# Kernel tuning notes

Hardware: AMD Instinct MI355X
Metric: run time of the kernel (lower is better)

The kernel has to match this reference:

```python
import jax, jax.numpy as jnp
import numpy as np

HIDDEN = 1024
N_EXPERTS = 8
TOP_K = 2
INTER = 1408
NORM_TOPK = False


def setup_inputs() -> dict:
    key = jax.random.key(0)
    ks = jax.random.split(key, 5)
    B, S = 4, 2048
    scale_h = 1.0 / np.sqrt(HIDDEN)
    scale_i = 1.0 / np.sqrt(INTER)
    return {
        "hidden_states": jax.random.normal(ks[0], (B, S, HIDDEN), dtype=jnp.float32),
        "gate_w": jax.random.normal(ks[1], (N_EXPERTS, HIDDEN), dtype=jnp.float32) * scale_h,  # router
        "w_gate": jax.random.normal(ks[2], (N_EXPERTS, HIDDEN, INTER), dtype=jnp.float32) * scale_h,
        "w_up": jax.random.normal(ks[3], (N_EXPERTS, HIDDEN, INTER), dtype=jnp.float32) * scale_h,
        "w_down": jax.random.normal(ks[4], (N_EXPERTS, INTER, HIDDEN), dtype=jnp.float32) * scale_i,
    }


def reference(hidden_states, gate_w, w_gate, w_up, w_down):
    B, S, H = hidden_states.shape
    x = hidden_states.reshape(-1, H)                     # [T, H]
    T = x.shape[0]

    router_logits = x @ gate_w.T                          # [T, E]
    probs = jax.nn.softmax(router_logits.astype(jnp.float32), axis=-1)
    topk_w, topk_idx = jax.lax.top_k(probs, TOP_K)        # [T, K]
    if NORM_TOPK:
        topk_w = topk_w / jnp.sum(topk_w, axis=-1, keepdims=True)
    topk_w = topk_w.astype(x.dtype)

    # Scatter top-k weights into dense [T, E] combine weights (0 for unselected).
    weights = jnp.zeros((T, N_EXPERTS), dtype=x.dtype)
    weights = weights.at[jnp.arange(T)[:, None], topk_idx].set(topk_w)

    # Dense grouped SwiGLU over all experts; combine masks out unrouted pairs.
    g = jnp.einsum('th,ehi->eti', x, w_gate)              # [E, T, I]
    u = jnp.einsum('th,ehi->eti', x, w_up)                # [E, T, I]
    y = jnp.einsum('eti,eih->eth', jax.nn.silu(g) * u, w_down)  # [E, T, H]
    final = jnp.einsum('eth,te->th', y, weights)          # [T, H]

    return final.reshape(B, S, H), router_logits
```

## Files before the change

kernel.cpp:

```cpp
#include <hip/hip_runtime.h>
#include <hip/hip_bf16.h>
#include <math.h>

#define T_TOK 8192
#define HID   1024
#define NE    8
#define TOPKN 2
#define INTER 1408
#define NROWS (T_TOK*TOPKN)
#define MAXWL256 72
#define RBLK  256
#define GX1   (INTER/128)
#define GX2   (HID/128)

typedef __attribute__((ext_vector_type(8))) __bf16 bf16x8;
typedef __attribute__((ext_vector_type(4))) float f32x4;
typedef __attribute__((ext_vector_type(4))) unsigned int u32x4;

__device__ __forceinline__ unsigned short f2bf(float f) {
    unsigned int u = __builtin_bit_cast(unsigned int, f);
    unsigned int lsb = (u >> 16) & 1u;
    u += 0x7fffu + lsb;
    return (unsigned short)(u >> 16);
}

__device__ __forceinline__ void gl2lds16(const void* g, void* l) {
    __builtin_amdgcn_global_load_lds(
        (const __attribute__((address_space(1))) unsigned int*)g,
        (__attribute__((address_space(3))) unsigned int*)l, 16, 0, 0);
}

__global__ __launch_bounds__(256) void moe_router(
    const float* __restrict__ x, const float* __restrict__ gate_w,
    unsigned short* __restrict__ xb, float* __restrict__ logits_out,
    int* __restrict__ topk_idx, float* __restrict__ topk_w,
    int* __restrict__ hist_g)
{
    __shared__ int lh[NE];
    int tid = threadIdx.x, wave = tid >> 6, lane = tid & 63;
    if (tid < NE) lh[tid] = 0;
    __syncthreads();

#pragma unroll 1
    for (int i = 0; i < 8; i++) {
        int t = blockIdx.x * 32 + wave * 8 + i;
        const float4* xr = (const float4*)(x + (size_t)t * HID);
        float acc[NE];
#pragma unroll
        for (int e = 0; e < NE; e++) acc[e] = 0.f;
#pragma unroll
        for (int j = 0; j < 4; j++) {
            float4 xv = xr[j * 64 + lane];
            ushort4 pk;
            pk.x = f2bf(xv.x); pk.y = f2bf(xv.y);
            pk.z = f2bf(xv.z); pk.w = f2bf(xv.w);
            *(ushort4*)(xb + (size_t)t * HID + j * 256 + lane * 4) = pk;
#pragma unroll
            for (int e = 0; e < NE; e++) {
                float4 gv = *(const float4*)(gate_w + e * HID + j * 256 + lane * 4);
                acc[e] += xv.x * gv.x + xv.y * gv.y + xv.z * gv.z + xv.w * gv.w;
            }
        }
#pragma unroll
        for (int e = 0; e < NE; e++) {
            float v = acc[e];
#pragma unroll
            for (int off = 32; off; off >>= 1) v += __shfl_xor(v, off, 64);
            acc[e] = v;
        }
        if (lane == 0) {
            float m = acc[0];
#pragma unroll
            for (int e = 1; e < NE; e++) m = fmaxf(m, acc[e]);
            float p[NE]; float s = 0.f;
#pragma unroll
            for (int e = 0; e < NE; e++) { p[e] = expf(acc[e] - m); s += p[e]; }
            float inv = 1.f / s;
#pragma unroll
            for (int e = 0; e < NE; e++) logits_out[(size_t)t * NE + e] = acc[e];
            int i0 = 0;
#pragma unroll
            for (int e = 1; e < NE; e++) if (p[e] > p[i0]) i0 = e;
            int i1 = (i0 == 0) ? 1 : 0;
#pragma unroll
            for (int e = 0; e < NE; e++) if (e != i0 && p[e] > p[i1]) i1 = e;
            topk_idx[2 * t]     = i0; topk_w[2 * t]     = p[i0] * inv;
            topk_idx[2 * t + 1] = i1; topk_w[2 * t + 1] = p[i1] * inv;
            atomicAdd(&lh[i0], 1);
            atomicAdd(&lh[i1], 1);
        }
    }
    __syncthreads();
    if (tid < NE) hist_g[blockIdx.x * NE + tid] = lh[tid];
}

__global__ __launch_bounds__(256) void moe_scan(
    const int* __restrict__ hist_g, int* __restrict__ offsets,
    int* __restrict__ block_base, int* __restrict__ wl256, int* __restrict__ n_wl256)
{
    __shared__ int h[RBLK * NE];
    __shared__ int cnt[NE], offs[NE];
    int tid = threadIdx.x;
    for (int i = tid; i < RBLK * NE; i += 256) h[i] = hist_g[i];
    __syncthreads();
    {
        int e = tid >> 5, g = tid & 31;
        int s = 0;
        for (int b = g; b < RBLK; b += 32) s += h[b * NE + e];
#pragma unroll
        for (int off2 = 16; off2; off2 >>= 1) s += __shfl_xor(s, off2, 32);
        if (g == 0) cnt[e] = s;
    }
    __syncthreads();
    if (tid == 0) {
        int s = 0;
        for (int e = 0; e < NE; e++) { offs[e] = s; offsets[e] = s; s += cnt[e]; }
        offsets[NE] = s;
        int n2 = 0;
        for (int e = 0; e < NE; e++)
            for (int r0 = 0; r0 < cnt[e]; r0 += 256)
                wl256[n2++] = (e << 24) | r0;
        *n_wl256 = n2;
    }
    __syncthreads();
    if (tid < NE) {
        int run = offs[tid];
        for (int b = 0; b < RBLK; b++) {
            block_base[b * NE + tid] = run;
            run += h[b * NE + tid];
        }
    }
}

__global__ __launch_bounds__(64) void moe_scatter(
    const int* __restrict__ topk_idx, const float* __restrict__ topk_w,
    const int* __restrict__ block_base, int* __restrict__ row_token,
    float* __restrict__ row_w, int* __restrict__ tok_rows)
{
    __shared__ int base[NE];
    int tid = threadIdx.x;
    if (tid < NE) base[tid] = block_base[blockIdx.x * NE + tid];
    __syncthreads();
    int idx = blockIdx.x * 64 + tid;
    int e = topk_idx[idx];
    int pos = atomicAdd(&base[e], 1);
    row_token[pos] = idx >> 1;
    row_w[pos] = topk_w[idx];
    tok_rows[idx] = pos;
}

__global__ __launch_bounds__(256) void moe_transpose_all(
    const float* __restrict__ w_gate, const float* __restrict__ w_up,
    const float* __restrict__ w_down,
    unsigned short* __restrict__ wg_t, unsigned short* __restrict__ wu_t,
    unsigned short* __restrict__ wd_t)
{
    __shared__ float tile[64][65];
    int z = blockIdx.y;
    int m = z >> 3, e = z & 7;
    const float* in; unsigned short* out; int R_, C_;
    if (m == 0)      { in = w_gate; out = wg_t; R_ = HID;   C_ = INTER; }
    else if (m == 1) { in = w_up;   out = wu_t; R_ = HID;   C_ = INTER; }
    else             { in = w_down; out = wd_t; R_ = INTER; C_ = HID;   }
    int ntx = C_ >> 6;
    int bx = (int)blockIdx.x % ntx, by = (int)blockIdx.x / ntx;
    const float* ine = in + (size_t)e * R_ * C_;
    unsigned short* oute = out + (size_t)e * R_ * C_;
    int c0 = bx * 64, r0 = by * 64;
    int tid = threadIdx.x;
    int lr = tid >> 4;
    int lc = tid & 15;
#pragma unroll
    for (int j = 0; j < 4; j++) {
        int r = lr + j * 16;
        float4 v = *(const float4*)(ine + (size_t)(r0 + r) * C_ + c0 + lc * 4);
        tile[r][lc * 4 + 0] = v.x; tile[r][lc * 4 + 1] = v.y;
        tile[r][lc * 4 + 2] = v.z; tile[r][lc * 4 + 3] = v.w;
    }
    __syncthreads();
#pragma unroll
    for (int j = 0; j < 4; j++) {
        int c = (tid >> 4) + j * 16;
        int r = (tid & 15) * 4;
        ushort4 pk;
        pk.x = f2bf(tile[r + 0][c]);
        pk.y = f2bf(tile[r + 1][c]);
        pk.z = f2bf(tile[r + 2][c]);
        pk.w = f2bf(tile[r + 3][c]);
        *(ushort4*)(oute + (size_t)(c0 + c) * R_ + r0 + r) = pk;
    }
}

__global__ __launch_bounds__(512, 2) void moe_gemm1(
    const unsigned short* __restrict__ xb,
    const unsigned short* __restrict__ wg_t,
    const unsigned short* __restrict__ wu_t,
    const int* __restrict__ offsets, const int* __restrict__ row_token,
    const int* __restrict__ wl, const int* __restrict__ n_wl,
    unsigned short* __restrict__ h_buf)
{
    if ((int)blockIdx.y >= *n_wl) return;
    int wle = wl[blockIdx.y];
    int e = wle >> 24, row0 = wle & 0xffffff;
    int off = offsets[e], cnt = offsets[e + 1] - off;
    int i0 = blockIdx.x * 128;

    __shared__ __align__(16) unsigned short As[32768];
    __shared__ __align__(16) unsigned short Bs[32768];

    int tid = threadIdx.x, wave = tid >> 6, lane = tid & 63;
    int wm = wave & 1, wn = wave >> 1;
    int l16 = lane & 15, quad = lane >> 4;
    int fsw = (l16 >> 1) & 3;

    int kswz = ((lane & 3) ^ ((lane >> 3) & 3)) * 8;
    int r0s = wave * 32 + (lane >> 2);
    int r1s = r0s + 16;

    int gA0 = row0 + r0s, gA1 = row0 + r1s;
    int tok0 = row_token[off + ((gA0 < cnt) ? gA0 : 0)];
    int tok1 = row_token[off + ((gA1 < cnt) ? gA1 : 0)];
    const unsigned short* aptr0 = xb + (size_t)tok0 * HID + kswz;
    const unsigned short* aptr1 = xb + (size_t)tok1 * HID + kswz;

    int ic0 = i0 + (r0s >> 6) * 32 + (r0s & 31);
    int ic1 = i0 + (r1s >> 6) * 32 + (r1s & 31);
    const unsigned short* bptr0 =
        (((r0s >> 5) & 1) ? wu_t : wg_t) + (size_t)e * INTER * HID + (size_t)ic0 * HID + kswz;
    const unsigned short* bptr1 =
        (((r1s >> 5) & 1) ? wu_t : wg_t) + (size_t)e * INTER * HID + (size_t)ic1 * HID + kswz;

    f32x4 acc[8][4];
#pragma unroll
    for (int mi = 0; mi < 8; mi++)
#pragma unroll
        for (int ni = 0; ni < 4; ni++) acc[mi][ni] = {0.f, 0.f, 0.f, 0.f};

    {
        unsigned short* dA = &As[wave * 1024];
        unsigned short* dB = &Bs[wave * 1024];
        gl2lds16(aptr0, dA);            gl2lds16(aptr1, dA + 512);
        gl2lds16(bptr0, dB);            gl2lds16(bptr1, dB + 512);
        gl2lds16(aptr0 + 32, dA + 8192); gl2lds16(aptr1 + 32, dA + 8192 + 512);
        gl2lds16(bptr0 + 32, dB + 8192); gl2lds16(bptr1 + 32, dB + 8192 + 512);
    }
    __syncthreads();

#pragma unroll 1
    for (int kt = 0; kt < 16; kt++) {
        const unsigned short* Ac = &As[(kt & 1) << 14];
        const unsigned short* Bc = &Bs[(kt & 1) << 14];
        unsigned short* An = &As[(((kt + 1) & 1) << 14) + wave * 1024];
        unsigned short* Bn = &Bs[(((kt + 1) & 1) << 14) + wave * 1024];
        int kb = (kt + 1) * 64;
        bool more = kt < 15;
        bf16x8 a[8], b0, b1;

        asm volatile("s_waitcnt vmcnt(4)" ::: "memory");
        __builtin_amdgcn_s_barrier();
#pragma unroll
        for (int mi = 0; mi < 8; mi++)
            a[mi] = *(const bf16x8*)&Ac[(wm * 128 + mi * 16 + l16) * 32 + (quad ^ fsw) * 8];
        b0 = *(const bf16x8*)&Bc[(wn * 64 + l16) * 32 + (quad ^ fsw) * 8];
        b1 = *(const bf16x8*)&Bc[(wn * 64 + 16 + l16) * 32 + (quad ^ fsw) * 8];
        if (more) { gl2lds16(aptr0 + kb, An); gl2lds16(aptr1 + kb, An + 512); }
        __builtin_amdgcn_s_setprio(1);
#pragma unroll
        for (int mi = 0; mi < 8; mi++) {
            acc[mi][0] = __builtin_amdgcn_mfma_f32_16x16x32_bf16(a[mi], b0, acc[mi][0], 0, 0, 0);
            acc[mi][1] = __builtin_amdgcn_mfma_f32_16x16x32_bf16(a[mi], b1, acc[mi][1], 0, 0, 0);
        }
        __builtin_amdgcn_s_setprio(0);

        asm volatile("s_waitcnt vmcnt(6)" ::: "memory");
        __builtin_amdgcn_s_barrier();
        b0 = *(const bf16x8*)&Bc[(wn * 64 + 32 + l16) * 32 + (quad ^ fsw) * 8];
        b1 = *(const bf16x8*)&Bc[(wn * 64 + 48 + l16) * 32 + (quad ^ fsw) * 8];
        if (more) { gl2lds16(bptr0 + kb, Bn); gl2lds16(bptr1 + kb, Bn + 512); }
        __builtin_amdgcn_s_setprio(1);
#pragma unroll
        for (int mi = 0; mi < 8; mi++) {
            acc[mi][2] = __builtin_amdgcn_mfma_f32_16x16x32_bf16(a[mi], b0, acc[mi][2], 0, 0, 0);
            acc[mi][3] = __builtin_amdgcn_mfma_f32_16x16x32_bf16(a[mi], b1, acc[mi][3], 0, 0, 0);
        }
        __builtin_amdgcn_s_setprio(0);

        asm volatile("s_waitcnt vmcnt(4)" ::: "memory");
        __builtin_amdgcn_s_barrier();
#pragma unroll
        for (int mi = 0; mi < 8; mi++)
            a[mi] = *(const bf16x8*)&Ac[8192 + (wm * 128 + mi * 16 + l16) * 32 + (quad ^ fsw) * 8];
        b0 = *(const bf16x8*)&Bc[8192 + (wn * 64 + l16) * 32 + (quad ^ fsw) * 8];
        b1 = *(const bf16x8*)&Bc[8192 + (wn * 64 + 16 + l16) * 32 + (quad ^ fsw) * 8];
        if (more) { gl2lds16(aptr0 + kb + 32, An + 8192); gl2lds16(aptr1 + kb + 32, An + 8192 + 512); }
        __builtin_amdgcn_s_setprio(1);
#pragma unroll
        for (int mi = 0; mi < 8; mi++) {
            acc[mi][0] = __builtin_amdgcn_mfma_f32_16x16x32_bf16(a[mi], b0, acc[mi][0], 0, 0, 0);
            acc[mi][1] = __builtin_amdgcn_mfma_f32_16x16x32_bf16(a[mi], b1, acc[mi][1], 0, 0, 0);
        }
        __builtin_amdgcn_s_setprio(0);

        asm volatile("s_waitcnt vmcnt(6)" ::: "memory");
        __builtin_amdgcn_s_barrier();
        b0 = *(const bf16x8*)&Bc[8192 + (wn * 64 + 32 + l16) * 32 + (quad ^ fsw) * 8];
        b1 = *(const bf16x8*)&Bc[8192 + (wn * 64 + 48 + l16) * 32 + (quad ^ fsw) * 8];
        if (more) { gl2lds16(bptr0 + kb + 32, Bn + 8192); gl2lds16(bptr1 + kb + 32, Bn + 8192 + 512); }
        __builtin_amdgcn_s_setprio(1);
#pragma unroll
        for (int mi = 0; mi < 8; mi++) {
            acc[mi][2] = __builtin_amdgcn_mfma_f32_16x16x32_bf16(a[mi], b0, acc[mi][2], 0, 0, 0);
            acc[mi][3] = __builtin_amdgcn_mfma_f32_16x16x32_bf16(a[mi], b1, acc[mi][3], 0, 0, 0);
        }
        __builtin_amdgcn_s_setprio(0);
    }

#pragma unroll
    for (int mi = 0; mi < 8; mi++)
#pragma unroll
        for (int np = 0; np < 2; np++)
#pragma unroll
            for (int r = 0; r < 4; r++) {
                int ml = wm * 128 + mi * 16 + quad * 4 + r;
                int row = row0 + ml;
                if (row < cnt) {
                    float g = acc[mi][np][r], u = acc[mi][np + 2][r];
                    float hv = (g / (1.f + expf(-g))) * u;
                    h_buf[(size_t)(off + row) * INTER + i0 + wn * 32 + np * 16 + l16] = f2bf(hv);
                }
            }
}

__global__ __launch_bounds__(512, 2) void moe_gemm2(
    const unsigned short* __restrict__ h_buf,
    const unsigned short* __restrict__ wd_t,
    const int* __restrict__ offsets, const float* __restrict__ row_w,
    const int* __restrict__ wl, const int* __restrict__ n_wl,
    unsigned short* __restrict__ y_buf)
{
    if ((int)blockIdx.y >= *n_wl) return;
    int wle = wl[blockIdx.y];
    int e = wle >> 24, row0 = wle & 0xffffff;
    int off = offsets[e], cnt = offsets[e + 1] - off;
    int h0 = blockIdx.x * 128;

    __shared__ __align__(16) unsigned short As[32768];
    __shared__ __align__(16) unsigned short Bs[16384];

    int tid = threadIdx.x, wave = tid >> 6, lane = tid & 63;
    int wm = wave & 1, wn = wave >> 1;
    int l16 = lane & 15, quad = lane >> 4;
    int fsw = (l16 >> 1) & 3;

    int kswz = ((lane & 3) ^ ((lane >> 3) & 3)) * 8;
    int r0s = wave * 32 + (lane >> 2);
    int r1s = r0s + 16;
    int rbs = wave * 16 + (lane >> 2);

    int gA0 = row0 + r0s, gA1 = row0 + r1s;
    const unsigned short* aptr0 = h_buf + (size_t)(off + ((gA0 < cnt) ? gA0 : 0)) * INTER + kswz;
    const unsigned short* aptr1 = h_buf + (size_t)(off + ((gA1 < cnt) ? gA1 : 0)) * INTER + kswz;
    const unsigned short* bptr  = wd_t + (size_t)e * HID * INTER + (size_t)(h0 + rbs) * INTER + kswz;

    f32x4 acc[8][2];
#pragma unroll
    for (int mi = 0; mi < 8; mi++)
#pragma unroll
        for (int ni = 0; ni < 2; ni++) acc[mi][ni] = {0.f, 0.f, 0.f, 0.f};

    {
        unsigned short* dA = &As[wave * 1024];
        unsigned short* dB = &Bs[wave * 512];
        gl2lds16(aptr0, dA);             gl2lds16(aptr1, dA + 512);
        gl2lds16(bptr, dB);
        gl2lds16(aptr0 + 32, dA + 8192); gl2lds16(aptr1 + 32, dA + 8192 + 512);
        gl2lds16(bptr + 32, dB + 4096);
    }
    __syncthreads();

#pragma unroll 1
    for (int kt = 0; kt < 22; kt++) {
        const unsigned short* Ac = &As[(kt & 1) << 14];
        const unsigned short* Bc = &Bs[(kt & 1) << 13];
        unsigned short* An = &As[(((kt + 1) & 1) << 14) + wave * 1024];
        unsigned short* Bn = &Bs[(((kt + 1) & 1) << 13) + wave * 512];
        int kb = (kt + 1) * 64;
        bool more = kt < 21;
        bf16x8 a[8], b0, b1;

        asm volatile("s_waitcnt vmcnt(3)" ::: "memory");
        __builtin_amdgcn_s_barrier();
#pragma unroll
        for (int mi = 0; mi < 8; mi++)
            a[mi] = *(const bf16x8*)&Ac[(wm * 128 + mi * 16 + l16) * 32 + (quad ^ fsw) * 8];
        b0 = *(const bf16x8*)&Bc[(wn * 32 + l16) * 32 + (quad ^ fsw) * 8];
        b1 = *(const bf16x8*)&Bc[(wn * 32 + 16 + l16) * 32 + (quad ^ fsw) * 8];
        if (more) {
            gl2lds16(aptr0 + kb, An); gl2lds16(aptr1 + kb, An + 512);
            gl2lds16(bptr + kb, Bn);
        }
        __builtin_amdgcn_s_setprio(1);
#pragma unroll
        for (int mi = 0; mi < 8; mi++) {
            acc[mi][0] = __builtin_amdgcn_mfma_f32_16x16x32_bf16(a[mi], b0, acc[mi][0], 0, 0, 0);
            acc[mi][1] = __builtin_amdgcn_mfma_f32_16x16x32_bf16(a[mi], b1, acc[mi][1], 0, 0, 0);
        }
        __builtin_amdgcn_s_setprio(0);

        asm volatile("s_waitcnt vmcnt(3)" ::: "memory");
        __builtin_amdgcn_s_barrier();
#pragma unroll
        for (int mi = 0; mi < 8; mi++)
            a[mi] = *(const bf16x8*)&Ac[8192 + (wm * 128 + mi * 16 + l16) * 32 + (quad ^ fsw) * 8];
        b0 = *(const bf16x8*)&Bc[4096 + (wn * 32 + l16) * 32 + (quad ^ fsw) * 8];
        b1 = *(const bf16x8*)&Bc[4096 + (wn * 32 + 16 + l16) * 32 + (quad ^ fsw) * 8];
        if (more) {
            gl2lds16(aptr0 + kb + 32, An + 8192); gl2lds16(aptr1 + kb + 32, An + 8192 + 512);
            gl2lds16(bptr + kb + 32, Bn + 4096);
        }
        __builtin_amdgcn_s_setprio(1);
#pragma unroll
        for (int mi = 0; mi < 8; mi++) {
            acc[mi][0] = __builtin_amdgcn_mfma_f32_16x16x32_bf16(a[mi], b0, acc[mi][0], 0, 0, 0);
            acc[mi][1] = __builtin_amdgcn_mfma_f32_16x16x32_bf16(a[mi], b1, acc[mi][1], 0, 0, 0);
        }
        __builtin_amdgcn_s_setprio(0);
    }

#pragma unroll
    for (int mi = 0; mi < 8; mi++)
#pragma unroll
        for (int ni = 0; ni < 2; ni++)
#pragma unroll
            for (int r = 0; r < 4; r++) {
                int ml = wm * 128 + mi * 16 + quad * 4 + r;
                int row = row0 + ml;
                if (row < cnt) {
                    float w = row_w[off + row];
                    y_buf[(size_t)(off + row) * HID + h0 + wn * 32 + ni * 16 + l16] =
                        f2bf(acc[mi][ni][r] * w);
                }
            }
}

__global__ __launch_bounds__(256) void moe_combine(
    const unsigned short* __restrict__ y_buf, const int* __restrict__ tok_rows,
    float* __restrict__ out)
{
    int gid = blockIdx.x * 256 + threadIdx.x;
    int t = gid >> 7;
    int c = gid & 127;
    u32x4 a = *(const u32x4*)(y_buf + (size_t)tok_rows[2 * t]     * HID + c * 8);
    u32x4 b = *(const u32x4*)(y_buf + (size_t)tok_rows[2 * t + 1] * HID + c * 8);
    float res[8];
#pragma unroll
    for (int j = 0; j < 4; j++) {
        unsigned int wa = a[j], wb = b[j];
        res[2 * j]     = __builtin_bit_cast(float, wa << 16)
                       + __builtin_bit_cast(float, wb << 16);
        res[2 * j + 1] = __builtin_bit_cast(float, wa & 0xffff0000u)
                       + __builtin_bit_cast(float, wb & 0xffff0000u);
    }
    float* o = out + (size_t)t * HID + c * 8;
    *(float4*)(o)     = make_float4(res[0], res[1], res[2], res[3]);
    *(float4*)(o + 4) = make_float4(res[4], res[5], res[6], res[7]);
}

extern "C" void kernel_launch(void* const* d_in, const int* in_sizes, int n_in,
                              void* d_out, int out_size, void* d_ws, size_t ws_size,
                              hipStream_t stream)
{
    const float* x      = (const float*)d_in[0];
    const float* gate_w = (const float*)d_in[1];
    const float* w_gate = (const float*)d_in[2];
    const float* w_up   = (const float*)d_in[3];
    const float* w_down = (const float*)d_in[4];
    float* out = (float*)d_out;
    float* logits_out = out + (size_t)T_TOK * HID;

    char* ws = (char*)d_ws;
    int*   offsets    = (int*)(ws + 0);
    int*   n_wl256    = (int*)(ws + 68);
    int*   wl256      = (int*)(ws + 704);
    int*   hist_g     = (int*)(ws + 1024);
    int*   block_base = (int*)(ws + 1024 + 8192);
    int*   topk_idx   = (int*)(ws + 32768);
    float* topk_w     = (float*)(ws + 32768 + 65536);
    int*   row_token  = (int*)(ws + 32768 + 2 * 65536);
    float* row_w      = (float*)(ws + 32768 + 3 * 65536);
    int*   tok_rows   = (int*)(ws + 32768 + 4 * 65536);
    size_t o = 32768 + 5 * (size_t)65536 + 32768;
    unsigned short* xb   = (unsigned short*)(ws + o); o += (size_t)T_TOK * HID * 2;
    unsigned short* wg_t = (unsigned short*)(ws + o); o += (size_t)NE * INTER * HID * 2;
    unsigned short* wu_t = (unsigned short*)(ws + o); o += (size_t)NE * INTER * HID * 2;
    unsigned short* wd_t = (unsigned short*)(ws + o); o += (size_t)NE * HID * INTER * 2;
    unsigned short* h_buf = (unsigned short*)(ws + o); o += (size_t)NROWS * INTER * 2;
    unsigned short* y_buf = (unsigned short*)(ws + o); o += (size_t)NROWS * HID * 2;

    moe_router<<<RBLK, 256, 0, stream>>>(x, gate_w, xb, logits_out,
                                         topk_idx, topk_w, hist_g);
    moe_scan<<<1, 256, 0, stream>>>(hist_g, offsets, block_base, wl256, n_wl256);
    moe_scatter<<<RBLK, 64, 0, stream>>>(topk_idx, topk_w, block_base,
                                         row_token, row_w, tok_rows);
    moe_transpose_all<<<dim3(352, 24), 256, 0, stream>>>(
        w_gate, w_up, w_down, wg_t, wu_t, wd_t);

    moe_gemm1<<<dim3(GX1, MAXWL256), 512, 0, stream>>>(
        xb, wg_t, wu_t, offsets, row_token, wl256, n_wl256, h_buf);
    moe_gemm2<<<dim3(GX2, MAXWL256), 512, 0, stream>>>(
        h_buf, wd_t, offsets, row_w, wl256, n_wl256, y_buf);
    moe_combine<<<(T_TOK * HID / 8) / 256, 256, 0, stream>>>(y_buf, tok_rows, out);
}
```

Before: 439.4 us.

## Fuse router with weight transpose, peel GEMM tails, retile down-proj GEMM to 128x128

Merges the router and the weight transpose/convert into one launch so the two independent jobs share the GPU and one launch is saved. Peels the last K iteration of both GEMMs so the steady-state loop no longer branches on whether to prefetch. Retiles the down-projection GEMM from 256-row, 512-thread blocks to 128x128 tiles with 256 threads, driven by a new 128-row work list built in the scan kernel. This gives more blocks and less padding waste on partial expert tiles, at the cost of less reuse per tile and more B traffic.

```diff
diff --git a/kernel.cpp b/kernel.cpp
--- a/kernel.cpp
+++ b/kernel.cpp
@@ -9,9 +9,11 @@
 #define INTER 1408
 #define NROWS (T_TOK*TOPKN)
 #define MAXWL256 72
+#define MAXWL128 144
 #define RBLK  256
 #define GX1   (INTER/128)
 #define GX2   (HID/128)
+#define NTRT  8448
 
 typedef __attribute__((ext_vector_type(8))) __bf16 bf16x8;
 typedef __attribute__((ext_vector_type(4))) float f32x4;
@@ -30,73 +32,117 @@
         (__attribute__((address_space(3))) unsigned int*)l, 16, 0, 0);
 }
 
-__global__ __launch_bounds__(256) void moe_router(
+__global__ __launch_bounds__(256) void moe_pre(
     const float* __restrict__ x, const float* __restrict__ gate_w,
+    const float* __restrict__ w_gate, const float* __restrict__ w_up,
+    const float* __restrict__ w_down,
     unsigned short* __restrict__ xb, float* __restrict__ logits_out,
     int* __restrict__ topk_idx, float* __restrict__ topk_w,
-    int* __restrict__ hist_g)
-{
-    __shared__ int lh[NE];
-    int tid = threadIdx.x, wave = tid >> 6, lane = tid & 63;
-    if (tid < NE) lh[tid] = 0;
-    __syncthreads();
-
+    int* __restrict__ hist_g,
+    unsigned short* __restrict__ wg_t, unsigned short* __restrict__ wu_t,
+    unsigned short* __restrict__ wd_t)
+{
+    __shared__ float smem[64 * 65];
+    int tid = threadIdx.x;
+
+    if ((int)blockIdx.x < RBLK) {
+        int* lh = (int*)smem;
+        int wave = tid >> 6, lane = tid & 63;
+        if (tid < NE) lh[tid] = 0;
+        __syncthreads();
 #pragma unroll 1
-    for (int i = 0; i < 8; i++) {
-        int t = blockIdx.x * 32 + wave * 8 + i;
-        const float4* xr = (const float4*)(x + (size_t)t * HID);
-        float acc[NE];
-#pragma unroll
-        for (int e = 0; e < NE; e++) acc[e] = 0.f;
+        for (int i = 0; i < 8; i++) {
+            int t = blockIdx.x * 32 + wave * 8 + i;
+            const float4* xr = (const float4*)(x + (size_t)t * HID);
+            float acc[NE];
+#pragma unroll
+            for (int e = 0; e < NE; e++) acc[e] = 0.f;
+#pragma unroll
+            for (int j = 0; j < 4; j++) {
+                float4 xv = xr[j * 64 + lane];
+                ushort4 pk;
+                pk.x = f2bf(xv.x); pk.y = f2bf(xv.y);
+                pk.z = f2bf(xv.z); pk.w = f2bf(xv.w);
+                *(ushort4*)(xb + (size_t)t * HID + j * 256 + lane * 4) = pk;
+#pragma unroll
+                for (int e = 0; e < NE; e++) {
+                    float4 gv = *(const float4*)(gate_w + e * HID + j * 256 + lane * 4);
+                    acc[e] += xv.x * gv.x + xv.y * gv.y + xv.z * gv.z + xv.w * gv.w;
+                }
+            }
+#pragma unroll
+            for (int e = 0; e < NE; e++) {
+                float v = acc[e];
+#pragma unroll
+                for (int off = 32; off; off >>= 1) v += __shfl_xor(v, off, 64);
+                acc[e] = v;
+            }
+            if (lane == 0) {
+                float m = acc[0];
+#pragma unroll
+                for (int e = 1; e < NE; e++) m = fmaxf(m, acc[e]);
+                float p[NE]; float s = 0.f;
+#pragma unroll
+                for (int e = 0; e < NE; e++) { p[e] = expf(acc[e] - m); s += p[e]; }
+                float inv = 1.f / s;
+#pragma unroll
+                for (int e = 0; e < NE; e++) logits_out[(size_t)t * NE + e] = acc[e];
+                int i0 = 0;
+#pragma unroll
+                for (int e = 1; e < NE; e++) if (p[e] > p[i0]) i0 = e;
+                int i1 = (i0 == 0) ? 1 : 0;
+#pragma unroll
+                for (int e = 0; e < NE; e++) if (e != i0 && p[e] > p[i1]) i1 = e;
+                topk_idx[2 * t]     = i0; topk_w[2 * t]     = p[i0] * inv;
+                topk_idx[2 * t + 1] = i1; topk_w[2 * t + 1] = p[i1] * inv;
+                atomicAdd(&lh[i0], 1);
+                atomicAdd(&lh[i1], 1);
+            }
+        }
+        __syncthreads();
+        if (tid < NE) hist_g[blockIdx.x * NE + tid] = lh[tid];
+    } else {
+        int tz = (int)blockIdx.x - RBLK;
+        int z = tz / 352, txy = tz % 352;
+        int m = z >> 3, e = z & 7;
+        const float* in; unsigned short* out; int R_, C_;
+        if (m == 0)      { in = w_gate; out = wg_t; R_ = HID;   C_ = INTER; }
+        else if (m == 1) { in = w_up;   out = wu_t; R_ = HID;   C_ = INTER; }
+        else             { in = w_down; out = wd_t; R_ = INTER; C_ = HID;   }
+        int ntx = C_ >> 6;
+        int bx = txy % ntx, by = txy / ntx;
+        const float* ine = in + (size_t)e * R_ * C_;
+        unsigned short* oute = out + (size_t)e * R_ * C_;
+        int c0 = bx * 64, r0 = by * 64;
+        int lr = tid >> 4;
+        int lc = tid & 15;
 #pragma unroll
         for (int j = 0; j < 4; j++) {
-            float4 xv = xr[j * 64 + lane];
+            int r = lr + j * 16;
+            float4 v = *(const float4*)(ine + (size_t)(r0 + r) * C_ + c0 + lc * 4);
+            smem[r * 65 + lc * 4 + 0] = v.x; smem[r * 65 + lc * 4 + 1] = v.y;
+            smem[r * 65 + lc * 4 + 2] = v.z; smem[r * 65 + lc * 4 + 3] = v.w;
+        }
+        __syncthreads();
+#pragma unroll
+        for (int j = 0; j < 4; j++) {
+            int c = (tid >> 4) + j * 16;
+            int r = (tid & 15) * 4;
             ushort4 pk;
-            pk.x = f2bf(xv.x); pk.y = f2bf(xv.y);
-            pk.z = f2bf(xv.z); pk.w = f2bf(xv.w);
-            *(ushort4*)(xb + (size_t)t * HID + j * 256 + lane * 4) = pk;
-#pragma unroll
-            for (int e = 0; e < NE; e++) {
-                float4 gv = *(const float4*)(gate_w + e * HID + j * 256 + lane * 4);
-                acc[e] += xv.x * gv.x + xv.y * gv.y + xv.z * gv.z + xv.w * gv.w;
-            }
-        }
-#pragma unroll
-        for (int e = 0; e < NE; e++) {
-            float v = acc[e];
-#pragma unroll
-            for (int off = 32; off; off >>= 1) v += __shfl_xor(v, off, 64);
-            acc[e] = v;
-        }
-        if (lane == 0) {
-            float m = acc[0];
-#pragma unroll
-            for (int e = 1; e < NE; e++) m = fmaxf(m, acc[e]);
-            float p[NE]; float s = 0.f;
-#pragma unroll
-            for (int e = 0; e < NE; e++) { p[e] = expf(acc[e] - m); s += p[e]; }
-            float inv = 1.f / s;
-#pragma unroll
-            for (int e = 0; e < NE; e++) logits_out[(size_t)t * NE + e] = acc[e];
-            int i0 = 0;
-#pragma unroll
-            for (int e = 1; e < NE; e++) if (p[e] > p[i0]) i0 = e;
-            int i1 = (i0 == 0) ? 1 : 0;
-#pragma unroll
-            for (int e = 0; e < NE; e++) if (e != i0 && p[e] > p[i1]) i1 = e;
-            topk_idx[2 * t]     = i0; topk_w[2 * t]     = p[i0] * inv;
-            topk_idx[2 * t + 1] = i1; topk_w[2 * t + 1] = p[i1] * inv;
-            atomicAdd(&lh[i0], 1);
-            atomicAdd(&lh[i1], 1);
-        }
-    }
-    __syncthreads();
-    if (tid < NE) hist_g[blockIdx.x * NE + tid] = lh[tid];
+            pk.x = f2bf(smem[(r + 0) * 65 + c]);
+            pk.y = f2bf(smem[(r + 1) * 65 + c]);
+            pk.z = f2bf(smem[(r + 2) * 65 + c]);
+            pk.w = f2bf(smem[(r + 3) * 65 + c]);
+            *(ushort4*)(oute + (size_t)(c0 + c) * R_ + r0 + r) = pk;
+        }
+    }
 }
 
 __global__ __launch_bounds__(256) void moe_scan(
     const int* __restrict__ hist_g, int* __restrict__ offsets,
-    int* __restrict__ block_base, int* __restrict__ wl256, int* __restrict__ n_wl256)
+    int* __restrict__ block_base,
+    int* __restrict__ wl256, int* __restrict__ n_wl256,
+    int* __restrict__ wl128, int* __restrict__ n_wl128)
 {
     __shared__ int h[RBLK * NE];
     __shared__ int cnt[NE], offs[NE];
@@ -121,6 +167,11 @@
             for (int r0 = 0; r0 < cnt[e]; r0 += 256)
                 wl256[n2++] = (e << 24) | r0;
         *n_wl256 = n2;
+        int n1 = 0;
+        for (int e = 0; e < NE; e++)
+            for (int r0 = 0; r0 < cnt[e]; r0 += 128)
+                wl128[n1++] = (e << 24) | r0;
+        *n_wl128 = n1;
     }
     __syncthreads();
     if (tid < NE) {
@@ -149,48 +200,6 @@
     tok_rows[idx] = pos;
 }
 
-__global__ __launch_bounds__(256) void moe_transpose_all(
-    const float* __restrict__ w_gate, const float* __restrict__ w_up,
-    const float* __restrict__ w_down,
-    unsigned short* __restrict__ wg_t, unsigned short* __restrict__ wu_t,
-    unsigned short* __restrict__ wd_t)
-{
-    __shared__ float tile[64][65];
-    int z = blockIdx.y;
-    int m = z >> 3, e = z & 7;
-    const float* in; unsigned short* out; int R_, C_;
-    if (m == 0)      { in = w_gate; out = wg_t; R_ = HID;   C_ = INTER; }
-    else if (m == 1) { in = w_up;   out = wu_t; R_ = HID;   C_ = INTER; }
-    else             { in = w_down; out = wd_t; R_ = INTER; C_ = HID;   }
-    int ntx = C_ >> 6;
-    int bx = (int)blockIdx.x % ntx, by = (int)blockIdx.x / ntx;
-    const float* ine = in + (size_t)e * R_ * C_;
-    unsigned short* oute = out + (size_t)e * R_ * C_;
-    int c0 = bx * 64, r0 = by * 64;
-    int tid = threadIdx.x;
-    int lr = tid >> 4;
-    int lc = tid & 15;
-#pragma unroll
-    for (int j = 0; j < 4; j++) {
-        int r = lr + j * 16;
-        float4 v = *(const float4*)(ine + (size_t)(r0 + r) * C_ + c0 + lc * 4);
-        tile[r][lc * 4 + 0] = v.x; tile[r][lc * 4 + 1] = v.y;
-        tile[r][lc * 4 + 2] = v.z; tile[r][lc * 4 + 3] = v.w;
-    }
-    __syncthreads();
-#pragma unroll
-    for (int j = 0; j < 4; j++) {
-        int c = (tid >> 4) + j * 16;
-        int r = (tid & 15) * 4;
-        ushort4 pk;
-        pk.x = f2bf(tile[r + 0][c]);
-        pk.y = f2bf(tile[r + 1][c]);
-        pk.z = f2bf(tile[r + 2][c]);
-        pk.w = f2bf(tile[r + 3][c]);
-        *(ushort4*)(oute + (size_t)(c0 + c) * R_ + r0 + r) = pk;
-    }
-}
-
 __global__ __launch_bounds__(512, 2) void moe_gemm1(
     const unsigned short* __restrict__ xb,
     const unsigned short* __restrict__ wg_t,
@@ -247,13 +256,12 @@
     __syncthreads();
 
 #pragma unroll 1
-    for (int kt = 0; kt < 16; kt++) {
+    for (int kt = 0; kt < 15; kt++) {
         const unsigned short* Ac = &As[(kt & 1) << 14];
         const unsigned short* Bc = &Bs[(kt & 1) << 14];
         unsigned short* An = &As[(((kt + 1) & 1) << 14) + wave * 1024];
         unsigned short* Bn = &Bs[(((kt + 1) & 1) << 14) + wave * 1024];
         int kb = (kt + 1) * 64;
-        bool more = kt < 15;
         bf16x8 a[8], b0, b1;
 
         asm volatile("s_waitcnt vmcnt(4)" ::: "memory");
@@ -263,7 +271,7 @@
             a[mi] = *(const bf16x8*)&Ac[(wm * 128 + mi * 16 + l16) * 32 + (quad ^ fsw) * 8];
         b0 = *(const bf16x8*)&Bc[(wn * 64 + l16) * 32 + (quad ^ fsw) * 8];
         b1 = *(const bf16x8*)&Bc[(wn * 64 + 16 + l16) * 32 + (quad ^ fsw) * 8];
-        if (more) { gl2lds16(aptr0 + kb, An); gl2lds16(aptr1 + kb, An + 512); }
+        gl2lds16(aptr0 + kb, An); gl2lds16(aptr1 + kb, An + 512);
         __builtin_amdgcn_s_setprio(1);
 #pragma unroll
         for (int mi = 0; mi < 8; mi++) {
@@ -276,7 +284,7 @@
         __builtin_amdgcn_s_barrier();
         b0 = *(const bf16x8*)&Bc[(wn * 64 + 32 + l16) * 32 + (quad ^ fsw) * 8];
         b1 = *(const bf16x8*)&Bc[(wn * 64 + 48 + l16) * 32 + (quad ^ fsw) * 8];
-        if (more) { gl2lds16(bptr0 + kb, Bn); gl2lds16(bptr1 + kb, Bn + 512); }
+        gl2lds16(bptr0 + kb, Bn); gl2lds16(bptr1 + kb, Bn + 512);
         __builtin_amdgcn_s_setprio(1);
 #pragma unroll
         for (int mi = 0; mi < 8; mi++) {
@@ -292,7 +300,7 @@
             a[mi] = *(const bf16x8*)&Ac[8192 + (wm * 128 + mi * 16 + l16) * 32 + (quad ^ fsw) * 8];
         b0 = *(const bf16x8*)&Bc[8192 + (wn * 64 + l16) * 32 + (quad ^ fsw) * 8];
         b1 = *(const bf16x8*)&Bc[8192 + (wn * 64 + 16 + l16) * 32 + (quad ^ fsw) * 8];
-        if (more) { gl2lds16(aptr0 + kb + 32, An + 8192); gl2lds16(aptr1 + kb + 32, An + 8192 + 512); }
+        gl2lds16(aptr0 + kb + 32, An + 8192); gl2lds16(aptr1 + kb + 32, An + 8192 + 512);
         __builtin_amdgcn_s_setprio(1);
 #pragma unroll
         for (int mi = 0; mi < 8; mi++) {
@@ -305,7 +313,7 @@
         __builtin_amdgcn_s_barrier();
         b0 = *(const bf16x8*)&Bc[8192 + (wn * 64 + 32 + l16) * 32 + (quad ^ fsw) * 8];
         b1 = *(const bf16x8*)&Bc[8192 + (wn * 64 + 48 + l16) * 32 + (quad ^ fsw) * 8];
-        if (more) { gl2lds16(bptr0 + kb + 32, Bn + 8192); gl2lds16(bptr1 + kb + 32, Bn + 8192 + 512); }
+        gl2lds16(bptr0 + kb + 32, Bn + 8192); gl2lds16(bptr1 + kb + 32, Bn + 8192 + 512);
         __builtin_amdgcn_s_setprio(1);
 #pragma unroll
         for (int mi = 0; mi < 8; mi++) {
@@ -313,6 +321,35 @@
             acc[mi][3] = __builtin_amdgcn_mfma_f32_16x16x32_bf16(a[mi], b1, acc[mi][3], 0, 0, 0);
         }
         __builtin_amdgcn_s_setprio(0);
+    }
+
+    {
+        const unsigned short* Ac = &As[1 << 14];
+        const unsigned short* Bc = &Bs[1 << 14];
+        asm volatile("s_waitcnt vmcnt(0)" ::: "memory");
+        __builtin_amdgcn_s_barrier();
+        bf16x8 a[8], b0, b1;
+#pragma unroll
+        for (int sl = 0; sl < 2; sl++) {
+            int so = sl * 8192;
+#pragma unroll
+            for (int mi = 0; mi < 8; mi++)
+                a[mi] = *(const bf16x8*)&Ac[so + (wm * 128 + mi * 16 + l16) * 32 + (quad ^ fsw) * 8];
+            b0 = *(const bf16x8*)&Bc[so + (wn * 64 + l16) * 32 + (quad ^ fsw) * 8];
+            b1 = *(const bf16x8*)&Bc[so + (wn * 64 + 16 + l16) * 32 + (quad ^ fsw) * 8];
+#pragma unroll
+            for (int mi = 0; mi < 8; mi++) {
+                acc[mi][0] = __builtin_amdgcn_mfma_f32_16x16x32_bf16(a[mi], b0, acc[mi][0], 0, 0, 0);
+                acc[mi][1] = __builtin_amdgcn_mfma_f32_16x16x32_bf16(a[mi], b1, acc[mi][1], 0, 0, 0);
+            }
+            b0 = *(const bf16x8*)&Bc[so + (wn * 64 + 32 + l16) * 32 + (quad ^ fsw) * 8];
+            b1 = *(const bf16x8*)&Bc[so + (wn * 64 + 48 + l16) * 32 + (quad ^ fsw) * 8];
+#pragma unroll
+            for (int mi = 0; mi < 8; mi++) {
+                acc[mi][2] = __builtin_amdgcn_mfma_f32_16x16x32_bf16(a[mi], b0, acc[mi][2], 0, 0, 0);
+                acc[mi][3] = __builtin_amdgcn_mfma_f32_16x16x32_bf16(a[mi], b1, acc[mi][3], 0, 0, 0);
+            }
+        }
     }
 
 #pragma unroll
@@ -331,7 +368,7 @@
             }
 }
 
-__global__ __launch_bounds__(512, 2) void moe_gemm2(
+__global__ __launch_bounds__(256, 2) void moe_gemm2(
     const unsigned short* __restrict__ h_buf,
     const unsigned short* __restrict__ wd_t,
     const int* __restrict__ offsets, const float* __restrict__ row_w,
@@ -344,7 +381,7 @@
     int off = offsets[e], cnt = offsets[e + 1] - off;
     int h0 = blockIdx.x * 128;
 
-    __shared__ __align__(16) unsigned short As[32768];
+    __shared__ __align__(16) unsigned short As[16384];
     __shared__ __align__(16) unsigned short Bs[16384];
 
     int tid = threadIdx.x, wave = tid >> 6, lane = tid & 63;
@@ -353,91 +390,111 @@
     int fsw = (l16 >> 1) & 3;
 
     int kswz = ((lane & 3) ^ ((lane >> 3) & 3)) * 8;
-    int r0s = wave * 32 + (lane >> 2);
-    int r1s = r0s + 16;
-    int rbs = wave * 16 + (lane >> 2);
+    int r0s = wave * 16 + (lane >> 2);
+    int r1s = r0s + 64;
 
     int gA0 = row0 + r0s, gA1 = row0 + r1s;
     const unsigned short* aptr0 = h_buf + (size_t)(off + ((gA0 < cnt) ? gA0 : 0)) * INTER + kswz;
     const unsigned short* aptr1 = h_buf + (size_t)(off + ((gA1 < cnt) ? gA1 : 0)) * INTER + kswz;
-    const unsigned short* bptr  = wd_t + (size_t)e * HID * INTER + (size_t)(h0 + rbs) * INTER + kswz;
-
-    f32x4 acc[8][2];
-#pragma unroll
-    for (int mi = 0; mi < 8; mi++)
-#pragma unroll
-        for (int ni = 0; ni < 2; ni++) acc[mi][ni] = {0.f, 0.f, 0.f, 0.f};
+    const unsigned short* bptr0 = wd_t + (size_t)e * HID * INTER + (size_t)(h0 + r0s) * INTER + kswz;
+    const unsigned short* bptr1 = wd_t + (size_t)e * HID * INTER + (size_t)(h0 + r1s) * INTER + kswz;
+
+    f32x4 acc[4][4];
+#pragma unroll
+    for (int mi = 0; mi < 4; mi++)
+#pragma unroll
+        for (int ni = 0; ni < 4; ni++) acc[mi][ni] = {0.f, 0.f, 0.f, 0.f};
 
     {
-        unsigned short* dA = &As[wave * 1024];
+        unsigned short* dA = &As[wave * 512];
         unsigned short* dB = &Bs[wave * 512];
-        gl2lds16(aptr0, dA);             gl2lds16(aptr1, dA + 512);
-        gl2lds16(bptr, dB);
-        gl2lds16(aptr0 + 32, dA + 8192); gl2lds16(aptr1 + 32, dA + 8192 + 512);
-        gl2lds16(bptr + 32, dB + 4096);
+        gl2lds16(aptr0, dA);             gl2lds16(aptr1, dA + 2048);
+        gl2lds16(bptr0, dB);             gl2lds16(bptr1, dB + 2048);
+        gl2lds16(aptr0 + 32, dA + 4096); gl2lds16(aptr1 + 32, dA + 4096 + 2048);
+        gl2lds16(bptr0 + 32, dB + 4096); gl2lds16(bptr1 + 32, dB + 4096 + 2048);
     }
     __syncthreads();
 
 #pragma unroll 1
-    for (int kt = 0; kt < 22; kt++) {
-        const unsigned short* Ac = &As[(kt & 1) << 14];
+    for (int kt = 0; kt < 21; kt++) {
+        const unsigned short* Ac = &As[(kt & 1) << 13];
         const unsigned short* Bc = &Bs[(kt & 1) << 13];
-        unsigned short* An = &As[(((kt + 1) & 1) << 14) + wave * 1024];
+        unsigned short* An = &As[(((kt + 1) & 1) << 13) + wave * 512];
         unsigned short* Bn = &Bs[(((kt + 1) & 1) << 13) + wave * 512];
         int kb = (kt + 1) * 64;
-        bool more = kt < 21;
-        bf16x8 a[8], b0, b1;
-
-        asm volatile("s_waitcnt vmcnt(3)" ::: "memory");
-        __builtin_amdgcn_s_barrier();
-#pragma unroll
-        for (int mi = 0; mi < 8; mi++)
-            a[mi] = *(const bf16x8*)&Ac[(wm * 128 + mi * 16 + l16) * 32 + (quad ^ fsw) * 8];
-        b0 = *(const bf16x8*)&Bc[(wn * 32 + l16) * 32 + (quad ^ fsw) * 8];
-        b1 = *(const bf16x8*)&Bc[(wn * 32 + 16 + l16) * 32 + (quad ^ fsw) * 8];
-        if (more) {
-            gl2lds16(aptr0 + kb, An); gl2lds16(aptr1 + kb, An + 512);
-            gl2lds16(bptr + kb, Bn);
-        }
+        bf16x8 a[4], b[4];
+
+        asm volatile("s_waitcnt vmcnt(4)" ::: "memory");
+        __builtin_amdgcn_s_barrier();
+#pragma unroll
+        for (int mi = 0; mi < 4; mi++)
+            a[mi] = *(const bf16x8*)&Ac[(wm * 64 + mi * 16 + l16) * 32 + (quad ^ fsw) * 8];
+#pragma unroll
+        for (int ni = 0; ni < 4; ni++)
+            b[ni] = *(const bf16x8*)&Bc[(wn * 64 + ni * 16 + l16) * 32 + (quad ^ fsw) * 8];
+        gl2lds16(aptr0 + kb, An); gl2lds16(aptr1 + kb, An + 2048);
+        gl2lds16(bptr0 + kb, Bn); gl2lds16(bptr1 + kb, Bn + 2048);
         __builtin_amdgcn_s_setprio(1);
 #pragma unroll
-        for (int mi = 0; mi < 8; mi++) {
-            acc[mi][0] = __builtin_amdgcn_mfma_f32_16x16x32_bf16(a[mi], b0, acc[mi][0], 0, 0, 0);
-            acc[mi][1] = __builtin_amdgcn_mfma_f32_16x16x32_bf16(a[mi], b1, acc[mi][1], 0, 0, 0);
-        }
+        for (int mi = 0; mi < 4; mi++)
+#pragma unroll
+            for (int ni = 0; ni < 4; ni++)
+                acc[mi][ni] = __builtin_amdgcn_mfma_f32_16x16x32_bf16(a[mi], b[ni], acc[mi][ni], 0, 0, 0);
         __builtin_amdgcn_s_setprio(0);
 
-        asm volatile("s_waitcnt vmcnt(3)" ::: "memory");
-        __builtin_amdgcn_s_barrier();
-#pragma unroll
-        for (int mi = 0; mi < 8; mi++)
-            a[mi] = *(const bf16x8*)&Ac[8192 + (wm * 128 + mi * 16 + l16) * 32 + (quad ^ fsw) * 8];
-        b0 = *(const bf16x8*)&Bc[4096 + (wn * 32 + l16) * 32 + (quad ^ fsw) * 8];
-        b1 = *(const bf16x8*)&Bc[4096 + (wn * 32 + 16 + l16) * 32 + (quad ^ fsw) * 8];
-        if (more) {
-            gl2lds16(aptr0 + kb + 32, An + 8192); gl2lds16(aptr1 + kb + 32, An + 8192 + 512);
-            gl2lds16(bptr + kb + 32, Bn + 4096);
-        }
+        asm volatile("s_waitcnt vmcnt(4)" ::: "memory");
+        __builtin_amdgcn_s_barrier();
+#pragma unroll
+        for (int mi = 0; mi < 4; mi++)
+            a[mi] = *(const bf16x8*)&Ac[4096 + (wm * 64 + mi * 16 + l16) * 32 + (quad ^ fsw) * 8];
+#pragma unroll
+        for (int ni = 0; ni < 4; ni++)
+            b[ni] = *(const bf16x8*)&Bc[4096 + (wn * 64 + ni * 16 + l16) * 32 + (quad ^ fsw) * 8];
+        gl2lds16(aptr0 + kb + 32, An + 4096); gl2lds16(aptr1 + kb + 32, An + 4096 + 2048);
+        gl2lds16(bptr0 + kb + 32, Bn + 4096); gl2lds16(bptr1 + kb + 32, Bn + 4096 + 2048);
         __builtin_amdgcn_s_setprio(1);
 #pragma unroll
-        for (int mi = 0; mi < 8; mi++) {
-            acc[mi][0] = __builtin_amdgcn_mfma_f32_16x16x32_bf16(a[mi], b0, acc[mi][0], 0, 0, 0);
-            acc[mi][1] = __builtin_amdgcn_mfma_f32_16x16x32_bf16(a[mi], b1, acc[mi][1], 0, 0, 0);
-        }
+        for (int mi = 0; mi < 4; mi++)
+#pragma unroll
+            for (int ni = 0; ni < 4; ni++)
+                acc[mi][ni] = __builtin_amdgcn_mfma_f32_16x16x32_bf16(a[mi], b[ni], acc[mi][ni], 0, 0, 0);
         __builtin_amdgcn_s_setprio(0);
     }
 
-#pragma unroll
-    for (int mi = 0; mi < 8; mi++)
-#pragma unroll
-        for (int ni = 0; ni < 2; ni++)
+    {
+        const unsigned short* Ac = &As[1 << 13];
+        const unsigned short* Bc = &Bs[1 << 13];
+        asm volatile("s_waitcnt vmcnt(0)" ::: "memory");
+        __builtin_amdgcn_s_barrier();
+        bf16x8 a[4], b[4];
+#pragma unroll
+        for (int sl = 0; sl < 2; sl++) {
+            int so = sl * 4096;
+#pragma unroll
+            for (int mi = 0; mi < 4; mi++)
+                a[mi] = *(const bf16x8*)&Ac[so + (wm * 64 + mi * 16 + l16) * 32 + (quad ^ fsw) * 8];
+#pragma unroll
+            for (int ni = 0; ni < 4; ni++)
+                b[ni] = *(const bf16x8*)&Bc[so + (wn * 64 + ni * 16 + l16) * 32 + (quad ^ fsw) * 8];
+#pragma unroll
+            for (int mi = 0; mi < 4; mi++)
+#pragma unroll
+                for (int ni = 0; ni < 4; ni++)
+                    acc[mi][ni] = __builtin_amdgcn_mfma_f32_16x16x32_bf16(a[mi], b[ni], acc[mi][ni], 0, 0, 0);
+        }
+    }
+
+#pragma unroll
+    for (int mi = 0; mi < 4; mi++)
+#pragma unroll
+        for (int ni = 0; ni < 4; ni++)
 #pragma unroll
             for (int r = 0; r < 4; r++) {
-                int ml = wm * 128 + mi * 16 + quad * 4 + r;
+                int ml = wm * 64 + mi * 16 + quad * 4 + r;
                 int row = row0 + ml;
                 if (row < cnt) {
                     float w = row_w[off + row];
-                    y_buf[(size_t)(off + row) * HID + h0 + wn * 32 + ni * 16 + l16] =
+                    y_buf[(size_t)(off + row) * HID + h0 + wn * 64 + ni * 16 + l16] =
                         f2bf(acc[mi][ni][r] * w);
                 }
             }
@@ -480,10 +537,12 @@
 
     char* ws = (char*)d_ws;
     int*   offsets    = (int*)(ws + 0);
-    int*   n_wl256    = (int*)(ws + 68);
-    int*   wl256      = (int*)(ws + 704);
-    int*   hist_g     = (int*)(ws + 1024);
-    int*   block_base = (int*)(ws + 1024 + 8192);
+    int*   n_wl256    = (int*)(ws + 64);
+    int*   n_wl128    = (int*)(ws + 68);
+    int*   wl256      = (int*)(ws + 128);
+    int*   wl128      = (int*)(ws + 512);
+    int*   hist_g     = (int*)(ws + 2048);
+    int*   block_base = (int*)(ws + 2048 + 8192);
     int*   topk_idx   = (int*)(ws + 32768);
     float* topk_w     = (float*)(ws + 32768 + 65536);
     int*   row_token  = (int*)(ws + 32768 + 2 * 65536);
@@ -497,17 +556,17 @@
     unsigned short* h_buf = (unsigned short*)(ws + o); o += (size_t)NROWS * INTER * 2;
     unsigned short* y_buf = (unsigned short*)(ws + o); o += (size_t)NROWS * HID * 2;
 
-    moe_router<<<RBLK, 256, 0, stream>>>(x, gate_w, xb, logits_out,
-                                         topk_idx, topk_w, hist_g);
-    moe_scan<<<1, 256, 0, stream>>>(hist_g, offsets, block_base, wl256, n_wl256);
+    moe_pre<<<RBLK + NTRT, 256, 0, stream>>>(
+        x, gate_w, w_gate, w_up, w_down,
+        xb, logits_out, topk_idx, topk_w, hist_g, wg_t, wu_t, wd_t);
+    moe_scan<<<1, 256, 0, stream>>>(hist_g, offsets, block_base,
+                                    wl256, n_wl256, wl128, n_wl128);
     moe_scatter<<<RBLK, 64, 0, stream>>>(topk_idx, topk_w, block_base,
                                          row_token, row_w, tok_rows);
-    moe_transpose_all<<<dim3(352, 24), 256, 0, stream>>>(
-        w_gate, w_up, w_down, wg_t, wu_t, wd_t);
 
     moe_gemm1<<<dim3(GX1, MAXWL256), 512, 0, stream>>>(
         xb, wg_t, wu_t, offsets, row_token, wl256, n_wl256, h_buf);
-    moe_gemm2<<<dim3(GX2, MAXWL256), 512, 0, stream>>>(
-        h_buf, wd_t, offsets, row_w, wl256, n_wl256, y_buf);
+    moe_gemm2<<<dim3(GX2, MAXWL128), 256, 0, stream>>>(
+        h_buf, wd_t, offsets, row_w, wl128, n_wl128, y_buf);
     moe_combine<<<(T_TOK * HID / 8) / 256, 256, 0, stream>>>(y_buf, tok_rows, out);
 }
```

After: 433.0 us. Within noise of the previous version (-1.5%).
